# Kernel optimization log

Measured on AMD Instinct MI355X. Metric: run time of the kernel, lower is better.

## Reference

```python
import jax, jax.numpy as jnp
import numpy as np

SIZE = 7
SIGMA = 1.5
K1 = 0.01
K2 = 0.03
DATA_RANGE = 2.0
NP_ = SIZE * SIZE
COV_NORM = NP_ / (NP_ - 1)
PAD = SIZE // 2


def _gaussian_window(size=SIZE, sigma=SIGMA, channels=1):
    x = np.arange(size) - size // 2
    g = np.exp(-x**2 / (2.0 * sigma**2))[None, :]
    g = (g.T @ g)
    g = g / g.sum()
    w = np.tile(g[None, None], (channels, 1, 1, 1))  # [C,1,size,size]
    return jnp.asarray(w, dtype=jnp.float32)


def _dwconv(x, w):
    # depthwise conv2d, zero padding PAD, stride 1; x: [N,C,H,W], w: [C,1,k,k]
    c = x.shape[1]
    return jax.lax.conv_general_dilated(
        x, w, window_strides=(1, 1), padding=[(PAD, PAD), (PAD, PAD)],
        dimension_numbers=('NCHW', 'OIHW', 'NCHW'), feature_group_count=c)


def setup_inputs() -> dict:
    key = jax.random.key(0)
    k1, k2 = jax.random.split(key)
    X = jax.random.uniform(k1, (64, 1, 320, 320), dtype=jnp.float32)
    Y = jax.random.uniform(k2, (64, 1, 320, 320), dtype=jnp.float32)
    window = _gaussian_window()
    return {"X": X, "Y": Y, "window": window}


def reference(X, Y, window):
    C1 = (K1 * DATA_RANGE) ** 2
    C2 = (K2 * DATA_RANGE) ** 2
    mux = _dwconv(X, window)
    muy = _dwconv(Y, window)
    mux_sq = mux * mux
    muy_sq = muy * muy
    muxy = mux * muy
    sigmax_sq = (_dwconv(X * X, window) - mux_sq) * COV_NORM
    sigmay_sq = (_dwconv(Y * Y, window) - muy_sq) * COV_NORM
    sigmaxy = (_dwconv(X * Y, window) - muxy) * COV_NORM
    ssim_map = ((2 * muxy + C1) * (2 * sigmaxy + C2)) / \
               ((mux_sq + muy_sq + C1) * (sigmax_sq + sigmay_sq + C2))
    return 1.0 - ssim_map.mean()
```

## Files before the change

kernel.cpp:

```cpp
#include <hip/hip_runtime.h>
#include <math.h>


#define WI 320
#define HI 320
#define NI 64
#define TW 64
#define TH 16
#define GXD 5
#define GYD 20
#define NBLK (GXD * GYD * NI)
#define LSTR 72
#define NPIX ((double)NI * WI * HI)

typedef float v4 __attribute__((ext_vector_type(4)));

struct W7 { float w[7]; };

template <bool YI, bool XI>
__device__ __forceinline__ void column_task(
    const float* __restrict__ Xn, const float* __restrict__ Yn,
    const W7& wv, float* __restrict__ vbuf, int tx0, int ty0, int band, int ci)
{
    const int gx   = tx0 + ci - 3;
    const bool xok = XI || ((unsigned)gx < (unsigned)WI);
    const int gy0  = ty0 + band * 4 - 3;

    float xr[10], yr[10];
#pragma unroll
    for (int j = 0; j < 10; ++j) {
        const int gy  = gy0 + j;
        const bool ok = xok && (YI || ((unsigned)gy < (unsigned)HI));
        float xv = 0.f, yv = 0.f;
        if (ok) {
            const int idx = gy * WI + gx;
            xv = Xn[idx];
            yv = Yn[idx];
        }
        xr[j] = xv;
        yr[j] = yv;
    }

    float acc[5][4];
#pragma unroll
    for (int ch = 0; ch < 5; ++ch)
#pragma unroll
        for (int r = 0; r < 4; ++r) acc[ch][r] = 0.f;

#pragma unroll
    for (int j = 0; j < 10; ++j) {
        const float xv = xr[j], yv = yr[j];
        const float pxx = xv * xv, pyy = yv * yv, pxy = xv * yv;
#pragma unroll
        for (int r = 0; r < 4; ++r) {
            const int d = j - r;
            if (d >= 0 && d < 7) {
                const float w = wv.w[d];
                acc[0][r] += w * xv;
                acc[1][r] += w * yv;
                acc[2][r] += w * pxx;
                acc[3][r] += w * pyy;
                acc[4][r] += w * pxy;
            }
        }
    }
#pragma unroll
    for (int ch = 0; ch < 5; ++ch)
#pragma unroll
        for (int r = 0; r < 4; ++r)
            vbuf[ch * (TH * LSTR) + (band * 4 + r) * LSTR + ci] = acc[ch][r];
}

__global__ __launch_bounds__(320) void ssim_kernel(
    const float* __restrict__ X, const float* __restrict__ Y,
    W7 wv, float* __restrict__ partial)
{
    __shared__ __align__(16) float vbuf[5 * TH * LSTR];
    __shared__ float wsum[5];

    const int tid = threadIdx.x;
    const int tx0 = blockIdx.x * TW;
    const int ty0 = blockIdx.y * TH;
    const float* __restrict__ Xn = X + (size_t)blockIdx.z * (WI * HI);
    const float* __restrict__ Yn = Y + (size_t)blockIdx.z * (WI * HI);

    const bool yi = (blockIdx.y >= 1) && (blockIdx.y <= GYD - 2);
    const bool xi = (blockIdx.x >= 1) && (blockIdx.x <= GXD - 2);
    if (tid < 280) {
        int band, ci;
        if (tid < 256) { band = tid >> 6; ci = tid & 63; }
        else           { const int e = tid - 256; band = e / 6; ci = 64 + e % 6; }
        if (yi) {
            if (xi) column_task<true, true >(Xn, Yn, wv, vbuf, tx0, ty0, band, ci);
            else    column_task<true, false>(Xn, Yn, wv, vbuf, tx0, ty0, band, ci);
        } else {
            if (xi) column_task<false, true >(Xn, Yn, wv, vbuf, tx0, ty0, band, ci);
            else    column_task<false, false>(Xn, Yn, wv, vbuf, tx0, ty0, band, ci);
        }
    }
    __syncthreads();

    float lsum = 0.f;
    if (tid < 256) {
        const float C1 = 0.0004f, C2 = 0.0036f, COVN = 49.f / 48.f;
        const int row = tid >> 4;
        const int xg  = (tid & 15) << 2;

        float m[4][5];
#pragma unroll
        for (int j = 0; j < 4; ++j)
#pragma unroll
            for (int ch = 0; ch < 5; ++ch) m[j][ch] = 0.f;

#pragma unroll
        for (int ch = 0; ch < 5; ++ch) {
            const v4* p = (const v4*)&vbuf[ch * (TH * LSTR) + row * LSTR + xg];
            v4 a = p[0], b = p[1], c = p[2];
            float f[12] = {a.x,a.y,a.z,a.w, b.x,b.y,b.z,b.w, c.x,c.y,c.z,c.w};
#pragma unroll
            for (int j = 0; j < 4; ++j) {
                float s = 0.f;
#pragma unroll
                for (int d = 0; d < 7; ++d) s += wv.w[d] * f[j + d];
                m[j][ch] = s;
            }
        }
#pragma unroll
        for (int j = 0; j < 4; ++j) {
            const float mx = m[j][0], my = m[j][1];
            const float mxsq = mx * mx;
            const float mysq = my * my;
            const float mxy  = mx * my;
            const float vx   = (m[j][2] - mxsq) * COVN;
            const float vy   = (m[j][3] - mysq) * COVN;
            const float vxy  = (m[j][4] - mxy)  * COVN;
            const float num  = (2.f * mxy + C1) * (2.f * vxy + C2);
            const float den  = (mxsq + mysq + C1) * (vx + vy + C2);
            lsum += num * __builtin_amdgcn_rcpf(den);
        }
    }

#pragma unroll
    for (int off = 32; off > 0; off >>= 1)
        lsum += __shfl_down(lsum, off, 64);
    if ((tid & 63) == 0) wsum[tid >> 6] = lsum;
    __syncthreads();
    if (tid == 0) {
        int bid = (blockIdx.z * GYD + blockIdx.y) * GXD + blockIdx.x;
        partial[bid] = ((wsum[0] + wsum[1]) + (wsum[2] + wsum[3])) + wsum[4];
    }
}

__global__ __launch_bounds__(256) void ssim_finalize(
    const float* __restrict__ partial, float* __restrict__ out)
{
    __shared__ double ws[4];
    const int tid = threadIdx.x;
    double s = 0.0;
    for (int i = tid; i < NBLK; i += 256) s += (double)partial[i];
#pragma unroll
    for (int off = 32; off > 0; off >>= 1)
        s += __shfl_down(s, off, 64);
    if ((tid & 63) == 0) ws[tid >> 6] = s;
    __syncthreads();
    if (tid == 0)
        out[0] = (float)(1.0 - ((ws[0] + ws[1]) + (ws[2] + ws[3])) / NPIX);
}

extern "C" void kernel_launch(void* const* d_in, const int* in_sizes, int n_in,
                              void* d_out, int out_size, void* d_ws, size_t ws_size,
                              hipStream_t stream) {
    const float* X = (const float*)d_in[0];
    const float* Y = (const float*)d_in[1];
    W7 wv;
    {
        double g[7], s = 0.0;
        for (int i = 0; i < 7; ++i) {
            double x = (double)(i - 3);
            g[i] = exp(-(x * x) / (2.0 * 1.5 * 1.5));
            s += g[i];
        }
        for (int i = 0; i < 7; ++i) wv.w[i] = (float)(g[i] / s);
    }

    float* partial = (float*)d_ws;

    dim3 grid(GXD, GYD, NI);
    ssim_kernel<<<grid, 320, 0, stream>>>(X, Y, wv, partial);
    ssim_finalize<<<1, 256, 0, stream>>>(partial, (float*)d_out);
}
```

Baseline: 114.3 us.

## Make each wave own an independent overlapping tile strip, dropping block barrier

Restructures the SSIM kernel so each 64-lane wave computes a 4-row by 64-column vertical-pass strip in its own shared-memory slice and then runs the horizontal pass on it. Only a wave barrier is used, and the 320-thread block with a separate halo-column group is dropped. Tiles now step by 58 output columns with a 6-wide halo recomputed per wave, so the grid grows to 6 blocks in x. This removes the mid-kernel block-wide sync and the idle fifth wave, in exchange for about 10% redundant loads and compute plus masked lanes in the horizontal pass.

Measured after the change: 110.8 us. 1.03x faster.

```diff
diff --git a/kernel.cpp b/kernel.cpp
--- a/kernel.cpp
+++ b/kernel.cpp
@@ -5,40 +5,33 @@
 #define WI 320
 #define HI 320
 #define NI 64
-#define TW 64
-#define TH 16
-#define GXD 5
+#define TWO 58
+#define GXD 6
 #define GYD 20
 #define NBLK (GXD * GYD * NI)
-#define LSTR 72
 #define NPIX ((double)NI * WI * HI)
+#define WREG (5 * 4 * 64)
 
 typedef float v4 __attribute__((ext_vector_type(4)));
 
 struct W7 { float w[7]; };
 
-template <bool YI, bool XI>
-__device__ __forceinline__ void column_task(
+template <bool YI, int XM>
+__device__ __forceinline__ float wave_task(
     const float* __restrict__ Xn, const float* __restrict__ Yn,
-    const W7& wv, float* __restrict__ vbuf, int tx0, int ty0, int band, int ci)
+    const W7& wv, float* __restrict__ vb, int x0, int y0, int lane)
 {
-    const int gx   = tx0 + ci - 3;
-    const bool xok = XI || ((unsigned)gx < (unsigned)WI);
-    const int gy0  = ty0 + band * 4 - 3;
+    const int gx   = x0 + lane - 3;
+    const bool xok = (XM == 1) || (XM == 0 ? (gx >= 0) : (gx < WI));
 
     float xr[10], yr[10];
 #pragma unroll
     for (int j = 0; j < 10; ++j) {
-        const int gy  = gy0 + j;
+        const int gy  = y0 + j - 3;
         const bool ok = xok && (YI || ((unsigned)gy < (unsigned)HI));
         float xv = 0.f, yv = 0.f;
-        if (ok) {
-            const int idx = gy * WI + gx;
-            xv = Xn[idx];
-            yv = Yn[idx];
-        }
-        xr[j] = xv;
-        yr[j] = yv;
+        if (ok) { const int idx = gy * WI + gx; xv = Xn[idx]; yv = Yn[idx]; }
+        xr[j] = xv; yr[j] = yv;
     }
 
     float acc[5][4];
@@ -46,7 +39,6 @@
     for (int ch = 0; ch < 5; ++ch)
 #pragma unroll
         for (int r = 0; r < 4; ++r) acc[ch][r] = 0.f;
-
 #pragma unroll
     for (int j = 0; j < 10; ++j) {
         const float xv = xr[j], yv = yr[j];
@@ -68,53 +60,23 @@
     for (int ch = 0; ch < 5; ++ch)
 #pragma unroll
         for (int r = 0; r < 4; ++r)
-            vbuf[ch * (TH * LSTR) + (band * 4 + r) * LSTR + ci] = acc[ch][r];
-}
+            vb[ch * 256 + r * 64 + lane] = acc[ch][r];
 
-__global__ __launch_bounds__(320) void ssim_kernel(
-    const float* __restrict__ X, const float* __restrict__ Y,
-    W7 wv, float* __restrict__ partial)
-{
-    __shared__ __align__(16) float vbuf[5 * TH * LSTR];
-    __shared__ float wsum[5];
-
-    const int tid = threadIdx.x;
-    const int tx0 = blockIdx.x * TW;
-    const int ty0 = blockIdx.y * TH;
-    const float* __restrict__ Xn = X + (size_t)blockIdx.z * (WI * HI);
-    const float* __restrict__ Yn = Y + (size_t)blockIdx.z * (WI * HI);
-
-    const bool yi = (blockIdx.y >= 1) && (blockIdx.y <= GYD - 2);
-    const bool xi = (blockIdx.x >= 1) && (blockIdx.x <= GXD - 2);
-    if (tid < 280) {
-        int band, ci;
-        if (tid < 256) { band = tid >> 6; ci = tid & 63; }
-        else           { const int e = tid - 256; band = e / 6; ci = 64 + e % 6; }
-        if (yi) {
-            if (xi) column_task<true, true >(Xn, Yn, wv, vbuf, tx0, ty0, band, ci);
-            else    column_task<true, false>(Xn, Yn, wv, vbuf, tx0, ty0, band, ci);
-        } else {
-            if (xi) column_task<false, true >(Xn, Yn, wv, vbuf, tx0, ty0, band, ci);
-            else    column_task<false, false>(Xn, Yn, wv, vbuf, tx0, ty0, band, ci);
-        }
-    }
-    __syncthreads();
+    __builtin_amdgcn_wave_barrier();
 
     float lsum = 0.f;
-    if (tid < 256) {
+    const int row = lane >> 4;
+    const int xg  = (lane & 15) << 2;
+    if (xg < TWO) {
         const float C1 = 0.0004f, C2 = 0.0036f, COVN = 49.f / 48.f;
-        const int row = tid >> 4;
-        const int xg  = (tid & 15) << 2;
-
         float m[4][5];
 #pragma unroll
         for (int j = 0; j < 4; ++j)
 #pragma unroll
             for (int ch = 0; ch < 5; ++ch) m[j][ch] = 0.f;
-
 #pragma unroll
         for (int ch = 0; ch < 5; ++ch) {
-            const v4* p = (const v4*)&vbuf[ch * (TH * LSTR) + row * LSTR + xg];
+            const v4* p = (const v4*)&vb[ch * 256 + row * 64 + xg];
             v4 a = p[0], b = p[1], c = p[2];
             float f[12] = {a.x,a.y,a.z,a.w, b.x,b.y,b.z,b.w, c.x,c.y,c.z,c.w};
 #pragma unroll
@@ -136,18 +98,51 @@
             const float vxy  = (m[j][4] - mxy)  * COVN;
             const float num  = (2.f * mxy + C1) * (2.f * vxy + C2);
             const float den  = (mxsq + mysq + C1) * (vx + vy + C2);
-            lsum += num * __builtin_amdgcn_rcpf(den);
+            const bool valid = (xg + j < TWO) && (XM != 2 || x0 + xg + j < WI);
+            lsum += valid ? num * __builtin_amdgcn_rcpf(den) : 0.f;
         }
+    }
+    return lsum;
+}
+
+__global__ __launch_bounds__(256) void ssim_kernel(
+    const float* __restrict__ X, const float* __restrict__ Y,
+    W7 wv, float* __restrict__ partial)
+{
+    __shared__ __align__(16) float vbuf[4 * WREG + 16];
+    __shared__ float wsum[4];
+
+    const int tid  = threadIdx.x;
+    const int lane = tid & 63;
+    const int w    = tid >> 6;
+    const int x0   = blockIdx.x * TWO;
+    const int y0   = blockIdx.y * 16 + w * 4;
+    const float* __restrict__ Xn = X + (size_t)blockIdx.z * (WI * HI);
+    const float* __restrict__ Yn = Y + (size_t)blockIdx.z * (WI * HI);
+    float* vb = vbuf + w * WREG;
+
+    const bool yi = (y0 >= 3) && (y0 <= HI - 7);
+    const int  xm = (blockIdx.x == 0) ? 0 : ((blockIdx.x == GXD - 1) ? 2 : 1);
+
+    float lsum;
+    if (yi) {
+        if      (xm == 0) lsum = wave_task<true, 0>(Xn, Yn, wv, vb, x0, y0, lane);
+        else if (xm == 1) lsum = wave_task<true, 1>(Xn, Yn, wv, vb, x0, y0, lane);
+        else              lsum = wave_task<true, 2>(Xn, Yn, wv, vb, x0, y0, lane);
+    } else {
+        if      (xm == 0) lsum = wave_task<false, 0>(Xn, Yn, wv, vb, x0, y0, lane);
+        else if (xm == 1) lsum = wave_task<false, 1>(Xn, Yn, wv, vb, x0, y0, lane);
+        else              lsum = wave_task<false, 2>(Xn, Yn, wv, vb, x0, y0, lane);
     }
 
 #pragma unroll
     for (int off = 32; off > 0; off >>= 1)
         lsum += __shfl_down(lsum, off, 64);
-    if ((tid & 63) == 0) wsum[tid >> 6] = lsum;
+    if (lane == 0) wsum[w] = lsum;
     __syncthreads();
     if (tid == 0) {
-        int bid = (blockIdx.z * GYD + blockIdx.y) * GXD + blockIdx.x;
-        partial[bid] = ((wsum[0] + wsum[1]) + (wsum[2] + wsum[3])) + wsum[4];
+        const int bid = (blockIdx.z * GYD + blockIdx.y) * GXD + blockIdx.x;
+        partial[bid] = (wsum[0] + wsum[1]) + (wsum[2] + wsum[3]);
     }
 }
 
@@ -186,6 +181,6 @@
     float* partial = (float*)d_ws;
 
     dim3 grid(GXD, GYD, NI);
-    ssim_kernel<<<grid, 320, 0, stream>>>(X, Y, wv, partial);
+    ssim_kernel<<<grid, 256, 0, stream>>>(X, Y, wv, partial);
     ssim_finalize<<<1, 256, 0, stream>>>(partial, (float*)d_out);
 }
```
